# Kernel optimization log

Hardware: AMD Instinct MI355X
Metric: run time of the kernel (lower is better)

## Reference

```python
import jax, jax.numpy as jnp
import numpy as np

EPS = 1e-5  # torch LayerNorm default


def setup_inputs() -> dict:
    key = jax.random.key(0)
    ks = jax.random.split(key, 12)
    N, D, F = 4096, 1024, 4096
    s = 1.0 / np.sqrt(D)
    sf = 1.0 / np.sqrt(F)
    return {
        "embeddings": jax.random.normal(ks[0], (N, D), dtype=jnp.float32),
        "Wq": jax.random.normal(ks[1], (D, D), dtype=jnp.float32) * s,
        "bq": jnp.zeros((D,), jnp.float32),
        "Wk": jax.random.normal(ks[2], (D, D), dtype=jnp.float32) * s,
        "bk": jnp.zeros((D,), jnp.float32),
        "Wv": jax.random.normal(ks[3], (D, D), dtype=jnp.float32) * s,
        "bv": jnp.zeros((D,), jnp.float32),
        "gamma": jnp.ones((D,), jnp.float32),
        "beta": jnp.zeros((D,), jnp.float32),
        "W1": jax.random.normal(ks[4], (D, F), dtype=jnp.float32) * s,
        "b1": jnp.zeros((F,), jnp.float32),
        "W2": jax.random.normal(ks[5], (F, D), dtype=jnp.float32) * sf,
        "b2": jnp.zeros((D,), jnp.float32),
    }


def reference(embeddings, Wq, bq, Wk, bk, Wv, bv, gamma, beta, W1, b1, W2, b2):
    N, D = embeddings.shape
    scale = jnp.sqrt(jnp.float32(D))  # embed_dim ** 0.5
    Q = embeddings @ Wq + bq          # [N, D]
    K = embeddings @ Wk + bk
    V = embeddings @ Wv + bv
    attn = (Q @ K.T) / scale          # [N, N]
    # causal mask: strictly upper triangle -> -inf
    causal = jnp.tril(jnp.ones((N, N), dtype=bool))
    attn = jnp.where(causal, attn, -jnp.inf)
    A = jax.nn.softmax(attn, axis=-1)
    attn_emb = A @ V                  # [N, D]  (dropout = identity at eval)
    # add & norm (LayerNorm over last dim)
    x = attn_emb + embeddings
    mu = jnp.mean(x, axis=-1, keepdims=True)
    var = jnp.mean((x - mu) ** 2, axis=-1, keepdims=True)
    x = (x - mu) / jnp.sqrt(var + EPS) * gamma + beta
    # FFN (no residual after ff in the original module)
    h = jax.nn.relu(x @ W1 + b1)
    return h @ W2 + b2
```

## Files before the change

### kernel.cpp

```cpp
#include <hip/hip_runtime.h>
#include <stdint.h>


using short8 = __attribute__((ext_vector_type(8))) short;
using f32x4  = __attribute__((ext_vector_type(4))) float;

__device__ __forceinline__ uint16_t f2bf(float f) {
  uint32_t u = __builtin_bit_cast(uint32_t, f);
  u += 0x7FFFu + ((u >> 16) & 1u);
  return (uint16_t)(u >> 16);
}

__device__ __forceinline__ void gload_lds16(const uint16_t* g, uint16_t* l) {
  __builtin_amdgcn_global_load_lds(
      (__attribute__((address_space(1))) void*)(void*)g,
      (__attribute__((address_space(3))) void*)l, 16, 0, 0);
}


__global__ __launch_bounds__(256) void gemm_bt(
    const uint16_t* __restrict__ A, const uint16_t* __restrict__ Bt,
    const float* __restrict__ bias, void* __restrict__ Cout,
    uint16_t* __restrict__ VtOut,
    int K, int lda, int ldb, int ldc,
    float scale, int out_bf16, int relu)
{
  constexpr int BK = 64;
  __shared__ uint16_t As[128 * BK];
  __shared__ uint16_t Bs[128 * BK];
  int bm = blockIdx.y, bn = blockIdx.x;

  int tid  = threadIdx.x;
  int lane = tid & 63;
  int wave = tid >> 6;
  int wm = (wave >> 1) * 64, wn = (wave & 1) * 64;
  int lr = lane & 15, quad = lane >> 4;

  const uint16_t *Ag[4], *Bg[4];
  uint16_t *Al[4], *Bl[4];
#pragma unroll
  for (int s = 0; s < 4; ++s) {
    int c = tid + 256 * s;
    int r = c >> 3, q = (c & 7) ^ (r & 7);
    Ag[s] = A  + (size_t)(bm * 128 + r) * lda + q * 8;
    Bg[s] = Bt + (size_t)(bn * 128 + r) * ldb + q * 8;
    Al[s] = As + c * 8;
    Bl[s] = Bs + c * 8;
  }

  f32x4 acc[4][4] = {};

  for (int k0 = 0; k0 < K; k0 += BK) {
    __syncthreads();
#pragma unroll
    for (int s = 0; s < 4; ++s) gload_lds16(Ag[s] + k0, Al[s]);
#pragma unroll
    for (int s = 0; s < 4; ++s) gload_lds16(Bg[s] + k0, Bl[s]);
    __syncthreads();
#pragma unroll
    for (int h = 0; h < 2; ++h) {
      short8 af[4], bfr[4];
      int cc = quad + 4 * h;
#pragma unroll
      for (int i = 0; i < 4; ++i) {
        int r = wm + i * 16 + lr;
        af[i] = *(const short8*)(&As[(r * 8 + (cc ^ (r & 7))) * 8]);
      }
#pragma unroll
      for (int j = 0; j < 4; ++j) {
        int r = wn + j * 16 + lr;
        bfr[j] = *(const short8*)(&Bs[(r * 8 + (cc ^ (r & 7))) * 8]);
      }
#pragma unroll
      for (int i = 0; i < 4; ++i)
#pragma unroll
        for (int j = 0; j < 4; ++j)
          acc[i][j] = __builtin_amdgcn_mfma_f32_16x16x32_bf16(af[i], bfr[j], acc[i][j], 0, 0, 0);
    }
  }

  int row0 = bm * 128 + wm + quad * 4;
  int col0 = bn * 128 + wn + lr;
#pragma unroll
  for (int j = 0; j < 4; ++j) {
    int col = col0 + j * 16;
    float bv = bias ? bias[col] : 0.0f;
#pragma unroll
    for (int i = 0; i < 4; ++i) {
#pragma unroll
      for (int r = 0; r < 4; ++r) {
        int row = row0 + i * 16 + r;
        float v = acc[i][j][r] * scale + bv;
        if (relu) v = fmaxf(v, 0.0f);
        if (VtOut && col >= 2048) {
          VtOut[(size_t)(col - 2048) * 4096 + row] = f2bf(v);
        } else {
          size_t idx = (size_t)row * ldc + col;
          if (out_bf16) ((uint16_t*)Cout)[idx] = f2bf(v);
          else          ((float*)Cout)[idx]    = v;
        }
      }
    }
  }
}

__global__ __launch_bounds__(256) void gemm_s(
    const uint16_t* __restrict__ Qm, const uint16_t* __restrict__ Km,
    uint16_t* __restrict__ Sb, float* __restrict__ lvec,
    int lda, int ldb, int ldc, float scale)
{
  constexpr int BK = 64;
  __shared__ uint16_t As[64 * BK];
  __shared__ uint16_t Bs[128 * BK];
  int t = blockIdx.x;
  int u = (int)sqrtf((float)t);
  while ((u + 1) * (u + 1) <= t) ++u;
  while (u * u > t) --u;
  int i64, bn;
  if (t < u * (u + 1)) { i64 = 2 * u - 1; bn = t - u * u; }
  else                 { i64 = 2 * u;     bn = t - u * (u + 1); }

  int tid  = threadIdx.x;
  int lane = tid & 63;
  int wave = tid >> 6;
  int wm = (wave >> 1) * 32, wn = (wave & 1) * 64;
  int lr = lane & 15, quad = lane >> 4;

  const uint16_t *Ag[2], *Bg[4];
  uint16_t *Al[2], *Bl[4];
#pragma unroll
  for (int s = 0; s < 2; ++s) {
    int c = tid + 256 * s;
    int r = c >> 3, q = (c & 7) ^ (r & 7);
    Ag[s] = Qm + (size_t)(i64 * 64 + r) * lda + q * 8;
    Al[s] = As + c * 8;
  }
#pragma unroll
  for (int s = 0; s < 4; ++s) {
    int c = tid + 256 * s;
    int r = c >> 3, q = (c & 7) ^ (r & 7);
    Bg[s] = Km + (size_t)(bn * 128 + r) * ldb + q * 8;
    Bl[s] = Bs + c * 8;
  }

  f32x4 acc[2][4] = {};

  for (int k0 = 0; k0 < 1024; k0 += BK) {
    __syncthreads();
#pragma unroll
    for (int s = 0; s < 2; ++s) gload_lds16(Ag[s] + k0, Al[s]);
#pragma unroll
    for (int s = 0; s < 4; ++s) gload_lds16(Bg[s] + k0, Bl[s]);
    __syncthreads();
#pragma unroll
    for (int h = 0; h < 2; ++h) {
      short8 af[2], bfr[4];
      int cc = quad + 4 * h;
#pragma unroll
      for (int i = 0; i < 2; ++i) {
        int r = wm + i * 16 + lr;
        af[i] = *(const short8*)(&As[(r * 8 + (cc ^ (r & 7))) * 8]);
      }
#pragma unroll
      for (int j = 0; j < 4; ++j) {
        int r = wn + j * 16 + lr;
        bfr[j] = *(const short8*)(&Bs[(r * 8 + (cc ^ (r & 7))) * 8]);
      }
#pragma unroll
      for (int i = 0; i < 2; ++i)
#pragma unroll
        for (int j = 0; j < 4; ++j)
          acc[i][j] = __builtin_amdgcn_mfma_f32_16x16x32_bf16(af[i], bfr[j], acc[i][j], 0, 0, 0);
    }
  }

  int row0 = i64 * 64 + wm + quad * 4;
  int col0 = bn * 128 + wn + lr;
#pragma unroll
  for (int i = 0; i < 2; ++i) {
#pragma unroll
    for (int r = 0; r < 4; ++r) {
      int row = row0 + i * 16 + r;
      float s = 0.0f;
#pragma unroll
      for (int j = 0; j < 4; ++j) {
        int col = col0 + j * 16;
        float v = (col <= row) ? __expf(acc[i][j][r] * scale) : 0.0f;
        Sb[(size_t)row * ldc + col] = f2bf(v);
        s += v;
      }
#pragma unroll
      for (int o = 8; o > 0; o >>= 1) s += __shfl_xor(s, o, 64);
      if (lr == 0) unsafeAtomicAdd(&lvec[row], s);
    }
  }
}

__global__ __launch_bounds__(256) void gemm_bt_n64(
    const uint16_t* __restrict__ A, const uint16_t* __restrict__ Bt,
    void* __restrict__ Cout,
    int K, int lda, int ldb, int ldc, int mode)
{
  constexpr int BK = 64;
  __shared__ uint16_t As[128 * BK];
  __shared__ uint16_t Bs[64 * BK];
  int bn = blockIdx.x, b = blockIdx.y;
  int bm, half = 0, klo = 0, khi = K;
  if (mode == 2) {
    int t = b >> 1; half = b & 1;
    bm = (t & 1) ? (t >> 1) : (31 - (t >> 1));
    int kmax = (bm + 1) << 7, mid = kmax >> 1;
    klo = half ? mid : 0; khi = half ? kmax : mid;
  } else {
    bm = b >> 1; half = b & 1;
    int mid = K >> 1; klo = half ? mid : 0; khi = half ? K : mid;
  }

  int tid  = threadIdx.x;
  int lane = tid & 63;
  int wave = tid >> 6;
  int wm = (wave & 1) * 64, wn = (wave >> 1) * 32;
  int lr = lane & 15, quad = lane >> 4;

  const uint16_t *Ag[4], *Bg[2];
  uint16_t *Al[4], *Bl[2];
#pragma unroll
  for (int s = 0; s < 4; ++s) {
    int c = tid + 256 * s;
    int r = c >> 3, q = (c & 7) ^ (r & 7);
    Ag[s] = A + (size_t)(bm * 128 + r) * lda + q * 8;
    Al[s] = As + c * 8;
  }
#pragma unroll
  for (int s = 0; s < 2; ++s) {
    int c = tid + 256 * s;
    int r = c >> 3, q = (c & 7) ^ (r & 7);
    Bg[s] = Bt + (size_t)(bn * 64 + r) * ldb + q * 8;
    Bl[s] = Bs + c * 8;
  }

  f32x4 acc[4][2] = {};

  for (int k0 = klo; k0 < khi; k0 += BK) {
    __syncthreads();
#pragma unroll
    for (int s = 0; s < 4; ++s) gload_lds16(Ag[s] + k0, Al[s]);
#pragma unroll
    for (int s = 0; s < 2; ++s) gload_lds16(Bg[s] + k0, Bl[s]);
    __syncthreads();
#pragma unroll
    for (int h = 0; h < 2; ++h) {
      short8 af[4], bfr[2];
      int cc = quad + 4 * h;
#pragma unroll
      for (int i = 0; i < 4; ++i) {
        int r = wm + i * 16 + lr;
        af[i] = *(const short8*)(&As[(r * 8 + (cc ^ (r & 7))) * 8]);
      }
#pragma unroll
      for (int j = 0; j < 2; ++j) {
        int r = wn + j * 16 + lr;
        bfr[j] = *(const short8*)(&Bs[(r * 8 + (cc ^ (r & 7))) * 8]);
      }
#pragma unroll
      for (int i = 0; i < 4; ++i)
#pragma unroll
        for (int j = 0; j < 2; ++j)
          acc[i][j] = __builtin_amdgcn_mfma_f32_16x16x32_bf16(af[i], bfr[j], acc[i][j], 0, 0, 0);
    }
  }

  int row0 = bm * 128 + wm + quad * 4;
  int col0 = bn * 64 + wn + lr;
  if (mode == 4) {
    float* Cw = (float*)Cout;
#pragma unroll
    for (int j = 0; j < 2; ++j)
#pragma unroll
      for (int i = 0; i < 4; ++i)
#pragma unroll
        for (int r = 0; r < 4; ++r) {
          size_t idx = (size_t)(row0 + i * 16 + r) * ldc + col0 + j * 16;
          unsafeAtomicAdd(&Cw[idx], acc[i][j][r]);
        }
  } else {
    float* Cw = (float*)Cout + (size_t)half * 4096 * ldc;
#pragma unroll
    for (int j = 0; j < 2; ++j)
#pragma unroll
      for (int i = 0; i < 4; ++i)
#pragma unroll
        for (int r = 0; r < 4; ++r) {
          size_t idx = (size_t)(row0 + i * 16 + r) * ldc + col0 + j * 16;
          Cw[idx] = acc[i][j][r];
        }
  }
}

__device__ __forceinline__ float block_sum(float v, float* red) {
#pragma unroll
  for (int o = 32; o > 0; o >>= 1) v += __shfl_xor(v, o, 64);
  if ((threadIdx.x & 63) == 0) red[threadIdx.x >> 6] = v;
  __syncthreads();
  v = red[0] + red[1] + red[2] + red[3];
  __syncthreads();
  return v;
}

__global__ __launch_bounds__(256) void add_layernorm(
    const float* __restrict__ P, const float* __restrict__ l,
    const float* __restrict__ emb, const float* __restrict__ gamma,
    const float* __restrict__ beta, uint16_t* __restrict__ xB)
{
  __shared__ float red[4];
  int i = blockIdx.x, tid = threadIdx.x;
  float inv_l = 1.0f / l[i];
  float4 a0 = ((const float4*)(P + (size_t)i * 1024))[tid];
  float4 a1 = ((const float4*)(P + 4194304 + (size_t)i * 1024))[tid];
  float4 b  = ((const float4*)(emb + (size_t)i * 1024))[tid];
  float x0 = (a0.x + a1.x) * inv_l + b.x, x1 = (a0.y + a1.y) * inv_l + b.y;
  float x2 = (a0.z + a1.z) * inv_l + b.z, x3 = (a0.w + a1.w) * inv_l + b.w;
  float mu = block_sum(x0 + x1 + x2 + x3, red) * (1.0f / 1024.0f);
  float d0 = x0 - mu, d1 = x1 - mu, d2 = x2 - mu, d3 = x3 - mu;
  float var = block_sum(d0 * d0 + d1 * d1 + d2 * d2 + d3 * d3, red) * (1.0f / 1024.0f);
  float rs = rsqrtf(var + 1e-5f);
  float4 g  = ((const float4*)gamma)[tid];
  float4 be = ((const float4*)beta)[tid];
  ushort4 o;
  o.x = f2bf(d0 * rs * g.x + be.x);
  o.y = f2bf(d1 * rs * g.y + be.y);
  o.z = f2bf(d2 * rs * g.z + be.z);
  o.w = f2bf(d3 * rs * g.w + be.w);
  ((ushort4*)(xB + (size_t)i * 1024))[tid] = o;
}

__global__ __launch_bounds__(256) void prep(
    const float* __restrict__ emb, const float* __restrict__ Wq,
    const float* __restrict__ Wk, const float* __restrict__ Wv,
    const float* __restrict__ W1, const float* __restrict__ W2,
    const float* __restrict__ bq, const float* __restrict__ bk,
    const float* __restrict__ bv, const float* __restrict__ b2,
    uint16_t* __restrict__ embB, uint16_t* __restrict__ WqkvT,
    uint16_t* __restrict__ W1T, uint16_t* __restrict__ W2T,
    float* __restrict__ bqkv, float* __restrict__ lvec,
    float* __restrict__ outInit)
{
  __shared__ float tile[32][33];
  int b = blockIdx.x, tid = threadIdx.x;
  if (b < 4096) {
    int idx = b * 256 + tid;
    float4 v = ((const float4*)emb)[idx];
    ushort4 o; o.x = f2bf(v.x); o.y = f2bf(v.y); o.z = f2bf(v.z); o.w = f2bf(v.w);
    ((ushort4*)embB)[idx] = o;
    return;
  }
  int tx = tid & 31, ty = tid >> 5;
  if (b < 7168) {
    int local = b - 4096;
    const float* in = (local < 1024) ? Wq : (local < 2048) ? Wk : Wv;
    uint16_t* o = WqkvT + (size_t)(local >> 10) * 1048576;
    int rem = local & 1023;
    int r0 = (rem >> 5) * 32, c0 = (rem & 31) * 32;
#pragma unroll
    for (int r = 0; r < 32; r += 8)
      tile[ty + r][tx] = in[(size_t)(r0 + ty + r) * 1024 + c0 + tx];
    __syncthreads();
#pragma unroll
    for (int r = 0; r < 32; r += 8)
      o[(size_t)(c0 + ty + r) * 1024 + r0 + tx] = f2bf(tile[tx][ty + r]);
    return;
  }
  if (b < 11264) {
    int local = b - 7168;
    int c0 = (local & 127) * 32, r0 = (local >> 7) * 32;
#pragma unroll
    for (int r = 0; r < 32; r += 8)
      tile[ty + r][tx] = W1[(size_t)(r0 + ty + r) * 4096 + c0 + tx];
    __syncthreads();
#pragma unroll
    for (int r = 0; r < 32; r += 8)
      W1T[(size_t)(c0 + ty + r) * 1024 + r0 + tx] = f2bf(tile[tx][ty + r]);
    return;
  }
  if (b < 15360) {
    int local = b - 11264;
    int c0 = (local & 31) * 32, r0 = (local >> 5) * 32;
#pragma unroll
    for (int r = 0; r < 32; r += 8)
      tile[ty + r][tx] = W2[(size_t)(r0 + ty + r) * 1024 + c0 + tx];
    __syncthreads();
#pragma unroll
    for (int r = 0; r < 32; r += 8)
      W2T[(size_t)(c0 + ty + r) * 4096 + r0 + tx] = f2bf(tile[tx][ty + r]);
    return;
  }
  if (b < 15372) {
    int i = (b - 15360) * 256 + tid;
    bqkv[i] = (i < 1024) ? bq[i] : (i < 2048) ? bk[i - 1024] : bv[i - 2048];
    return;
  }
  if (b == 15372) {
#pragma unroll
    for (int i = tid; i < 4096; i += 256) lvec[i] = 0.0f;
    return;
  }
  {
    int row = b - 15373;
    float4 bv4 = ((const float4*)b2)[tid];
    ((float4*)(outInit + (size_t)row * 1024))[tid] = bv4;
  }
}

extern "C" void kernel_launch(void* const* d_in, const int* in_sizes, int n_in,
                              void* d_out, int out_size, void* d_ws, size_t ws_size,
                              hipStream_t stream) {
  const float* emb   = (const float*)d_in[0];
  const float* Wq    = (const float*)d_in[1];
  const float* bq    = (const float*)d_in[2];
  const float* Wk    = (const float*)d_in[3];
  const float* bk    = (const float*)d_in[4];
  const float* Wv    = (const float*)d_in[5];
  const float* bv    = (const float*)d_in[6];
  const float* gamma = (const float*)d_in[7];
  const float* beta  = (const float*)d_in[8];
  const float* W1    = (const float*)d_in[9];
  const float* b1    = (const float*)d_in[10];
  const float* W2    = (const float*)d_in[11];
  const float* b2    = (const float*)d_in[12];

  char* w = (char*)d_ws;
  const size_t MB = 1ull << 20;
  uint16_t* embB  = (uint16_t*)(w + 0 * MB);
  uint16_t* WqkvT = (uint16_t*)(w + 8 * MB);
  uint16_t* W1T   = (uint16_t*)(w + 14 * MB);
  uint16_t* W2T   = (uint16_t*)(w + 22 * MB);
  float*    bqkv  = (float*)(w + 30 * MB);
  float*    lvec  = (float*)(w + 30 * MB + 65536);
  uint16_t* QKVb  = (uint16_t*)(w + 31 * MB);
  uint16_t* Vt    = (uint16_t*)(w + 55 * MB);
  uint16_t* xB    = (uint16_t*)(w + 0 * MB);
  uint16_t* hB    = (uint16_t*)(w + 63 * MB);
  uint16_t* Sb    = (uint16_t*)(w + 95 * MB);
  float*    Opart = (float*)(w + 63 * MB);

  prep<<<19469, 256, 0, stream>>>(emb, Wq, Wk, Wv, W1, W2, bq, bk, bv, b2,
                                  embB, WqkvT, W1T, W2T, bqkv, lvec,
                                  (float*)d_out);

  gemm_bt<<<dim3(24, 32), 256, 0, stream>>>(embB, WqkvT, bqkv, QKVb, Vt,
      1024, 1024, 1024, 3072, 1.0f, 1, 0);
  const uint16_t* Qb = QKVb;
  const uint16_t* Kb = QKVb + 1024;

  gemm_s<<<1056, 256, 0, stream>>>(Qb, Kb, Sb, lvec, 3072, 3072, 4096, 0.03125f);

  gemm_bt_n64<<<dim3(16, 64), 256, 0, stream>>>(Sb, Vt, Opart,
      4096, 4096, 4096, 1024, 2);

  add_layernorm<<<4096, 256, 0, stream>>>(Opart, lvec, emb, gamma, beta, xB);

  gemm_bt<<<dim3(32, 32), 256, 0, stream>>>(xB, W1T, b1, hB, nullptr,
      1024, 1024, 1024, 4096, 1.0f, 1, 1);

  gemm_bt_n64<<<dim3(16, 64), 256, 0, stream>>>(hB, W2T, d_out,
      4096, 4096, 4096, 1024, 4);
}
```

Measured before the change: 364.0 us.

## Use 128x128 tiles with fixed K-chunk split for causal PV GEMM, coalesce V transpose

Replaces the P·V GEMM, which used 128x64 tiles and split each row block's causal K range in half, with a dedicated kernel using 128x128 tiles. Each row block's K range is cut into fixed 1024-wide chunks, giving up to four partial outputs that the layernorm kernel sums. The QKV GEMM now transposes its V tiles through LDS and writes them with coalesced 16-byte stores instead of scattered 2-byte stores. The second FFN GEMM gets a specialized kernel with a 1D grid ordered column-major. The workspace layout moves to make room for the four partial buffers, which adds extra partial-sum reads in layernorm.

```diff
diff --git a/kernel.cpp b/kernel.cpp
--- a/kernel.cpp
+++ b/kernel.cpp
@@ -26,8 +26,9 @@
     float scale, int out_bf16, int relu)
 {
   constexpr int BK = 64;
-  __shared__ uint16_t As[128 * BK];
-  __shared__ uint16_t Bs[128 * BK];
+  __shared__ uint16_t smem[2 * 128 * BK];
+  uint16_t* As = smem;
+  uint16_t* Bs = smem + 128 * BK;
   int bm = blockIdx.y, bn = blockIdx.x;
 
   int tid  = threadIdx.x;
@@ -81,6 +82,33 @@
 
   int row0 = bm * 128 + wm + quad * 4;
   int col0 = bn * 128 + wn + lr;
+
+  if (VtOut && bn >= 16) {
+    __syncthreads();
+#pragma unroll
+    for (int j = 0; j < 4; ++j) {
+      int cl = wn + j * 16 + lr;
+      float bv = bias ? bias[bn * 128 + cl] : 0.0f;
+#pragma unroll
+      for (int i = 0; i < 4; ++i)
+#pragma unroll
+        for (int r = 0; r < 4; ++r) {
+          int rl = wm + quad * 4 + i * 16 + r;
+          smem[cl * 128 + ((rl + 8 * cl) & 127)] = f2bf(acc[i][j][r] * scale + bv);
+        }
+    }
+    __syncthreads();
+    int cl = tid >> 1, rb = (tid & 1) * 64;
+    uint16_t* dst = VtOut + (size_t)((bn - 16) * 128 + cl) * 4096 + bm * 128;
+#pragma unroll
+    for (int k = 0; k < 8; ++k) {
+      int rl = rb + k * 8;
+      short8 v = *(const short8*)(&smem[cl * 128 + ((rl + 8 * cl) & 127)]);
+      *(short8*)(dst + rl) = v;
+    }
+    return;
+  }
+
 #pragma unroll
   for (int j = 0; j < 4; ++j) {
     int col = col0 + j * 16;
@@ -92,13 +120,9 @@
         int row = row0 + i * 16 + r;
         float v = acc[i][j][r] * scale + bv;
         if (relu) v = fmaxf(v, 0.0f);
-        if (VtOut && col >= 2048) {
-          VtOut[(size_t)(col - 2048) * 4096 + row] = f2bf(v);
-        } else {
-          size_t idx = (size_t)row * ldc + col;
-          if (out_bf16) ((uint16_t*)Cout)[idx] = f2bf(v);
-          else          ((float*)Cout)[idx]    = v;
-        }
+        size_t idx = (size_t)row * ldc + col;
+        if (out_bf16) ((uint16_t*)Cout)[idx] = f2bf(v);
+        else          ((float*)Cout)[idx]    = v;
       }
     }
   }
@@ -196,25 +220,95 @@
   }
 }
 
-__global__ __launch_bounds__(256) void gemm_bt_n64(
+__global__ __launch_bounds__(256) void gemm_o(
+    const uint16_t* __restrict__ Sb, const uint16_t* __restrict__ Vt,
+    float* __restrict__ Opart)
+{
+  constexpr int BK = 64;
+  __shared__ uint16_t As[128 * BK];
+  __shared__ uint16_t Bs[128 * BK];
+  int id = blockIdx.x;
+  int bn = id / 80, p = id % 80;
+  int c, bm;
+  if      (p < 32) { c = 0; bm = p; }
+  else if (p < 56) { c = 1; bm = p - 24; }
+  else if (p < 72) { c = 2; bm = p - 40; }
+  else             { c = 3; bm = p - 48; }
+  int klo = c << 10;
+  int khi = (bm + 1) << 7; if (khi > ((c + 1) << 10)) khi = (c + 1) << 10;
+
+  int tid  = threadIdx.x;
+  int lane = tid & 63;
+  int wave = tid >> 6;
+  int wm = (wave >> 1) * 64, wn = (wave & 1) * 64;
+  int lr = lane & 15, quad = lane >> 4;
+
+  const uint16_t *Ag[4], *Bg[4];
+  uint16_t *Al[4], *Bl[4];
+#pragma unroll
+  for (int s = 0; s < 4; ++s) {
+    int cch = tid + 256 * s;
+    int r = cch >> 3, q = (cch & 7) ^ (r & 7);
+    Ag[s] = Sb + (size_t)(bm * 128 + r) * 4096 + q * 8;
+    Bg[s] = Vt + (size_t)(bn * 128 + r) * 4096 + q * 8;
+    Al[s] = As + cch * 8;
+    Bl[s] = Bs + cch * 8;
+  }
+
+  f32x4 acc[4][4] = {};
+
+  for (int k0 = klo; k0 < khi; k0 += BK) {
+    __syncthreads();
+#pragma unroll
+    for (int s = 0; s < 4; ++s) gload_lds16(Ag[s] + k0, Al[s]);
+#pragma unroll
+    for (int s = 0; s < 4; ++s) gload_lds16(Bg[s] + k0, Bl[s]);
+    __syncthreads();
+#pragma unroll
+    for (int h = 0; h < 2; ++h) {
+      short8 af[4], bfr[4];
+      int cc = quad + 4 * h;
+#pragma unroll
+      for (int i = 0; i < 4; ++i) {
+        int r = wm + i * 16 + lr;
+        af[i] = *(const short8*)(&As[(r * 8 + (cc ^ (r & 7))) * 8]);
+      }
+#pragma unroll
+      for (int j = 0; j < 4; ++j) {
+        int r = wn + j * 16 + lr;
+        bfr[j] = *(const short8*)(&Bs[(r * 8 + (cc ^ (r & 7))) * 8]);
+      }
+#pragma unroll
+      for (int i = 0; i < 4; ++i)
+#pragma unroll
+        for (int j = 0; j < 4; ++j)
+          acc[i][j] = __builtin_amdgcn_mfma_f32_16x16x32_bf16(af[i], bfr[j], acc[i][j], 0, 0, 0);
+    }
+  }
+
+  float* P = Opart + (size_t)c * 4194304;
+  int row0 = bm * 128 + wm + quad * 4;
+  int col0 = bn * 128 + wn + lr;
+#pragma unroll
+  for (int j = 0; j < 4; ++j)
+#pragma unroll
+    for (int i = 0; i < 4; ++i)
+#pragma unroll
+      for (int r = 0; r < 4; ++r)
+        P[(size_t)(row0 + i * 16 + r) * 1024 + col0 + j * 16] = acc[i][j][r];
+}
+
+__global__ __launch_bounds__(256) void gemm_ffn2(
     const uint16_t* __restrict__ A, const uint16_t* __restrict__ Bt,
-    void* __restrict__ Cout,
-    int K, int lda, int ldb, int ldc, int mode)
+    float* __restrict__ Cout)
 {
   constexpr int BK = 64;
   __shared__ uint16_t As[128 * BK];
   __shared__ uint16_t Bs[64 * BK];
-  int bn = blockIdx.x, b = blockIdx.y;
-  int bm, half = 0, klo = 0, khi = K;
-  if (mode == 2) {
-    int t = b >> 1; half = b & 1;
-    bm = (t & 1) ? (t >> 1) : (31 - (t >> 1));
-    int kmax = (bm + 1) << 7, mid = kmax >> 1;
-    klo = half ? mid : 0; khi = half ? kmax : mid;
-  } else {
-    bm = b >> 1; half = b & 1;
-    int mid = K >> 1; klo = half ? mid : 0; khi = half ? K : mid;
-  }
+  int id = blockIdx.x;
+  int bn = id >> 6, p = id & 63;
+  int bm = p >> 1, half = p & 1;
+  int klo = half ? 2048 : 0, khi = half ? 4096 : 2048;
 
   int tid  = threadIdx.x;
   int lane = tid & 63;
@@ -228,14 +322,14 @@
   for (int s = 0; s < 4; ++s) {
     int c = tid + 256 * s;
     int r = c >> 3, q = (c & 7) ^ (r & 7);
-    Ag[s] = A + (size_t)(bm * 128 + r) * lda + q * 8;
+    Ag[s] = A + (size_t)(bm * 128 + r) * 4096 + q * 8;
     Al[s] = As + c * 8;
   }
 #pragma unroll
   for (int s = 0; s < 2; ++s) {
     int c = tid + 256 * s;
     int r = c >> 3, q = (c & 7) ^ (r & 7);
-    Bg[s] = Bt + (size_t)(bn * 64 + r) * ldb + q * 8;
+    Bg[s] = Bt + (size_t)(bn * 64 + r) * 4096 + q * 8;
     Bl[s] = Bs + c * 8;
   }
 
@@ -272,29 +366,15 @@
 
   int row0 = bm * 128 + wm + quad * 4;
   int col0 = bn * 64 + wn + lr;
-  if (mode == 4) {
-    float* Cw = (float*)Cout;
-#pragma unroll
-    for (int j = 0; j < 2; ++j)
-#pragma unroll
-      for (int i = 0; i < 4; ++i)
-#pragma unroll
-        for (int r = 0; r < 4; ++r) {
-          size_t idx = (size_t)(row0 + i * 16 + r) * ldc + col0 + j * 16;
-          unsafeAtomicAdd(&Cw[idx], acc[i][j][r]);
-        }
-  } else {
-    float* Cw = (float*)Cout + (size_t)half * 4096 * ldc;
-#pragma unroll
-    for (int j = 0; j < 2; ++j)
-#pragma unroll
-      for (int i = 0; i < 4; ++i)
-#pragma unroll
-        for (int r = 0; r < 4; ++r) {
-          size_t idx = (size_t)(row0 + i * 16 + r) * ldc + col0 + j * 16;
-          Cw[idx] = acc[i][j][r];
-        }
-  }
+#pragma unroll
+  for (int j = 0; j < 2; ++j)
+#pragma unroll
+    for (int i = 0; i < 4; ++i)
+#pragma unroll
+      for (int r = 0; r < 4; ++r) {
+        size_t idx = (size_t)(row0 + i * 16 + r) * 1024 + col0 + j * 16;
+        unsafeAtomicAdd(&Cout[idx], acc[i][j][r]);
+      }
 }
 
 __device__ __forceinline__ float block_sum(float v, float* red) {
@@ -315,11 +395,15 @@
   __shared__ float red[4];
   int i = blockIdx.x, tid = threadIdx.x;
   float inv_l = 1.0f / l[i];
-  float4 a0 = ((const float4*)(P + (size_t)i * 1024))[tid];
-  float4 a1 = ((const float4*)(P + 4194304 + (size_t)i * 1024))[tid];
-  float4 b  = ((const float4*)(emb + (size_t)i * 1024))[tid];
-  float x0 = (a0.x + a1.x) * inv_l + b.x, x1 = (a0.y + a1.y) * inv_l + b.y;
-  float x2 = (a0.z + a1.z) * inv_l + b.z, x3 = (a0.w + a1.w) * inv_l + b.w;
+  int nc = (i >> 10) + 1;
+  float s0 = 0.0f, s1 = 0.0f, s2 = 0.0f, s3 = 0.0f;
+  for (int c = 0; c < nc; ++c) {
+    float4 a = ((const float4*)(P + (size_t)c * 4194304 + (size_t)i * 1024))[tid];
+    s0 += a.x; s1 += a.y; s2 += a.z; s3 += a.w;
+  }
+  float4 b = ((const float4*)(emb + (size_t)i * 1024))[tid];
+  float x0 = s0 * inv_l + b.x, x1 = s1 * inv_l + b.y;
+  float x2 = s2 * inv_l + b.z, x3 = s3 * inv_l + b.w;
   float mu = block_sum(x0 + x1 + x2 + x3, red) * (1.0f / 1024.0f);
   float d0 = x0 - mu, d1 = x1 - mu, d2 = x2 - mu, d3 = x3 - mu;
   float var = block_sum(d0 * d0 + d1 * d1 + d2 * d2 + d3 * d3, red) * (1.0f / 1024.0f);
@@ -438,10 +522,10 @@
   float*    lvec  = (float*)(w + 30 * MB + 65536);
   uint16_t* QKVb  = (uint16_t*)(w + 31 * MB);
   uint16_t* Vt    = (uint16_t*)(w + 55 * MB);
+  uint16_t* Sb    = (uint16_t*)(w + 63 * MB);
+  uint16_t* hB    = (uint16_t*)(w + 63 * MB);
+  float*    Opart = (float*)(w + 95 * MB);
   uint16_t* xB    = (uint16_t*)(w + 0 * MB);
-  uint16_t* hB    = (uint16_t*)(w + 63 * MB);
-  uint16_t* Sb    = (uint16_t*)(w + 95 * MB);
-  float*    Opart = (float*)(w + 63 * MB);
 
   prep<<<19469, 256, 0, stream>>>(emb, Wq, Wk, Wv, W1, W2, bq, bk, bv, b2,
                                   embB, WqkvT, W1T, W2T, bqkv, lvec,
@@ -454,14 +538,12 @@
 
   gemm_s<<<1056, 256, 0, stream>>>(Qb, Kb, Sb, lvec, 3072, 3072, 4096, 0.03125f);
 
-  gemm_bt_n64<<<dim3(16, 64), 256, 0, stream>>>(Sb, Vt, Opart,
-      4096, 4096, 4096, 1024, 2);
+  gemm_o<<<640, 256, 0, stream>>>(Sb, Vt, Opart);
 
   add_layernorm<<<4096, 256, 0, stream>>>(Opart, lvec, emb, gamma, beta, xB);
 
   gemm_bt<<<dim3(32, 32), 256, 0, stream>>>(xB, W1T, b1, hB, nullptr,
       1024, 1024, 1024, 4096, 1.0f, 1, 1);
 
-  gemm_bt_n64<<<dim3(16, 64), 256, 0, stream>>>(hB, W2T, d_out,
-      4096, 4096, 4096, 1024, 4);
-}
+  gemm_ffn2<<<1024, 256, 0, stream>>>(hB, W2T, (float*)d_out);
+}
```

Result: no change. 360.5 us (-1.0%).
